# Kernel tuning notes

Hardware: AMD Instinct MI355X
Metric: run time of the kernel (lower is better)

The kernel has to match this reference:

```python
import jax, jax.numpy as jnp
import numpy as np

B, N, NB, P = 4, 2048, 10, 5
BIG = 1.0e5  # fill value for non-positive gt grasps


def _build_grasps(approach, base, contacts, thickness):
    # approach/base/contacts: [B,N,3], thickness: [B,N] -> [B,N,4,4]
    cross = jnp.cross(approach, base)
    R = jnp.stack([base, cross, approach], axis=-1)            # columns: [base, cross, approach]
    t = contacts + thickness[..., None] * 0.5 * base           # [B,N,3]
    top = jnp.concatenate([R, t[..., None]], axis=-1)          # [B,N,3,4]
    bottom = jnp.broadcast_to(jnp.array([0.0, 0.0, 0.0, 1.0], top.dtype),
                              top.shape[:-2] + (1, 4))
    return jnp.concatenate([top, bottom], axis=-2)             # [B,N,4,4]


def _transform_cps(cp_h, grasps):
    # cp_h: [P,4], grasps: [B,N,4,4] -> transformed control points [B,N,P,3]
    # torch: matmul(control_points, grasps^T)[..., :3]
    return jnp.einsum('pk,bnjk->bnpj', cp_h, grasps)[..., :3]


def _pairwise_sq(a, b):
    # a: [B,Na,P,3], b: [B,Nb,P,3] -> [B,Na,Nb] = sum_{p,c} (a-b)^2
    af = a.reshape(a.shape[0], a.shape[1], -1)
    bf = b.reshape(b.shape[0], b.shape[1], -1)
    a2 = jnp.sum(af * af, axis=-1)
    b2 = jnp.sum(bf * bf, axis=-1)
    d = a2[:, :, None] + b2[:, None, :] - 2.0 * jnp.einsum('bnd,bmd->bnm', af, bf)
    return jnp.maximum(d, 0.0)


def _forward(grasp_dir_head, approach_dir_head, grasp_offset_head, pred_points,
             binary_score_pred, binary_score_head, dir_labels_pc_cam, offset_labels_pc,
             grasp_success_labels_pc, approach_labels_pc_cam, bin_vals, bin_weights,
             control_pts, sym_control_pts):
    succ = grasp_success_labels_pc                              # [B,N] in {0,1}
    pos_in_view = jnp.maximum(jnp.sum(succ, axis=1), 1.0)       # min_geom_loss_divisor = 1.0

    # bin_offsets=True: lookup bin value of argmax bin
    thickness_pred = bin_vals[jnp.argmax(grasp_offset_head, axis=2)]   # [B,N]
    thickness_gt = bin_vals[jnp.argmax(offset_labels_pc, axis=2)]      # [B,N]

    pred_grasps = _build_grasps(approach_dir_head, grasp_dir_head, pred_points, thickness_pred)
    gt_grasps = _build_grasps(approach_labels_pc_cam, dir_labels_pc_cam, pred_points, thickness_gt)
    mask4 = succ.astype(bool)[:, :, None, None]
    pos_gt_grasps = jnp.where(mask4, gt_grasps, jnp.full_like(gt_grasps, BIG))

    ones_col = jnp.ones((P, 1), dtype=control_pts.dtype)
    cp_h = jnp.concatenate([control_pts, ones_col], axis=1)      # [P,4]
    scp_h = jnp.concatenate([sym_control_pts, ones_col], axis=1)

    pred_cp = _transform_cps(cp_h, pred_grasps)                  # [B,N,P,3]
    gt_cp_pos = _transform_cps(cp_h, pos_gt_grasps)
    sym_gt_cp_pos = _transform_cps(scp_h, pos_gt_grasps)

    # pred -> gt ADD-S (top-k with k=1 == min over concat of the two [B,N,N])
    d1 = _pairwise_sq(pred_cp, gt_cp_pos)
    d2 = _pairwise_sq(pred_cp, sym_gt_cp_pos)
    best = jnp.min(jnp.minimum(d1, d2), axis=2)                  # [B,N]
    gate = jnp.minimum(jnp.sum(succ, axis=1, keepdims=True), 1.0)
    min_adds = gate * jnp.sqrt(best)
    adds_loss = jnp.mean(binary_score_pred[:, :, 0] * min_adds)

    # gt -> pred ADD-S with unmasked gt grasps + confidence gather
    gt_cp = _transform_cps(cp_h, gt_grasps)
    sym_gt_cp = _transform_cps(scp_h, gt_grasps)
    dg1 = _pairwise_sq(gt_cp, pred_cp)                           # [B,Ngt,Npred]
    dg2 = _pairwise_sq(sym_gt_cp, pred_cp)
    m1 = jnp.min(dg1, axis=2); i1 = jnp.argmin(dg1, axis=2)
    m2 = jnp.min(dg2, axis=2); i2 = jnp.argmin(dg2, axis=2)
    # torch: where(-m1 < -m2, sym_idcs, idcs) == pick sym when m2 < m1
    idcs = jnp.where(m2 < m1, i2, i1)                            # [B,N]
    min_g2p = jnp.minimum(m1, m2) * succ
    conf = jnp.take_along_axis(binary_score_pred[:, :, 0], idcs, axis=1)
    adds_loss_gt2pred = jnp.mean(jnp.sum(conf * min_g2p, axis=1) / pos_in_view)

    # direction cosine loss
    cos_d = 1.0 - jnp.sum(dir_labels_pc_cam * grasp_dir_head, axis=2)
    dir_cosine_loss = jnp.mean(jnp.sum(cos_d * succ, axis=1) / pos_in_view)

    # approach cosine loss against orthogonalized label
    proj = jnp.sum(grasp_dir_head * approach_labels_pc_cam, axis=2, keepdims=True)
    orthog = approach_labels_pc_cam - proj * grasp_dir_head
    orthog = orthog / jnp.maximum(jnp.linalg.norm(orthog, axis=2, keepdims=True), 1e-12)
    cos_a = 1.0 - jnp.sum(orthog * approach_dir_head, axis=2)
    approach_cosine_loss = jnp.mean(jnp.sum(cos_a * succ, axis=1) / pos_in_view)

    # per-bin sigmoid BCE offset loss, bin-weighted
    bce = (offset_labels_pc * jax.nn.softplus(-grasp_offset_head)
           + (1.0 - offset_labels_pc) * jax.nn.softplus(grasp_offset_head))
    off = jnp.mean(bin_weights[None, None, :] * bce, axis=2)
    offset_loss = jnp.mean(jnp.sum(off * succ, axis=1) / pos_in_view)

    # binary success score BCE
    s = succ[:, :, None]
    score_bce = (s * jax.nn.softplus(-binary_score_head)
                 + (1.0 - s) * jax.nn.softplus(binary_score_head))
    bin_ce_loss = jnp.mean(score_bce)

    total = (1.0 * dir_cosine_loss + 1.0 * bin_ce_loss + 1.0 * offset_loss
             + 1.0 * approach_cosine_loss + 10.0 * adds_loss + 1.0 * adds_loss_gt2pred)
    return total


def setup_inputs():
    key = jax.random.key(0)
    ks = jax.random.split(key, 14)
    unit = lambda x: x / jnp.linalg.norm(x, axis=-1, keepdims=True)
    grasp_dir_head = unit(jax.random.normal(ks[0], (B, N, 3), jnp.float32))
    approach_dir_head = unit(jax.random.normal(ks[1], (B, N, 3), jnp.float32))
    grasp_offset_head = jax.random.normal(ks[2], (B, N, NB), jnp.float32)
    pred_points = jax.random.normal(ks[3], (B, N, 3), jnp.float32) * 0.3
    binary_score_pred = jax.random.uniform(ks[4], (B, N, 1), jnp.float32)
    binary_score_head = jax.random.normal(ks[5], (B, N, 1), jnp.float32)
    dir_labels_pc_cam = unit(jax.random.normal(ks[6], (B, N, 3), jnp.float32))
    offset_labels_pc = jax.nn.one_hot(jax.random.randint(ks[7], (B, N), 0, NB), NB, dtype=jnp.float32)
    grasp_success_labels_pc = jnp.round(jax.random.uniform(ks[8], (B, N), jnp.float32))
    approach_labels_pc_cam = unit(jax.random.normal(ks[9], (B, N, 3), jnp.float32))
    bin_vals = jnp.sort(jax.random.uniform(ks[10], (NB,), jnp.float32) * 0.075)
    bin_weights = jax.random.uniform(ks[11], (NB,), jnp.float32) + 0.5
    control_pts = jax.random.normal(ks[12], (P, 3), jnp.float32) * 0.05
    sym_control_pts = control_pts[jnp.array([0, 1, 3, 2, 4])]  # finger-swapped (symmetric) gripper
    return {
        'grasp_dir_head': grasp_dir_head,
        'approach_dir_head': approach_dir_head,
        'grasp_offset_head': grasp_offset_head,
        'pred_points': pred_points,
        'binary_score_pred': binary_score_pred,
        'binary_score_head': binary_score_head,
        'dir_labels_pc_cam': dir_labels_pc_cam,
        'offset_labels_pc': offset_labels_pc,
        'grasp_success_labels_pc': grasp_success_labels_pc,
        'approach_labels_pc_cam': approach_labels_pc_cam,
        'bin_vals': bin_vals,
        'bin_weights': bin_weights,
        'control_pts': control_pts,
        'sym_control_pts': sym_control_pts,
    }


def reference(grasp_dir_head, approach_dir_head, grasp_offset_head, pred_points,
              binary_score_pred, binary_score_head, dir_labels_pc_cam, offset_labels_pc,
              grasp_success_labels_pc, approach_labels_pc_cam, bin_vals, bin_weights,
              control_pts, sym_control_pts):
    return _forward(grasp_dir_head, approach_dir_head, grasp_offset_head, pred_points,
                    binary_score_pred, binary_score_head, dir_labels_pc_cam, offset_labels_pc,
                    grasp_success_labels_pc, approach_labels_pc_cam, bin_vals, bin_weights,
                    control_pts, sym_control_pts)
```

## Files before the change

### kernel.cpp

```cpp
#include <hip/hip_runtime.h>

#define Bn 4
#define Nn 2048
#define NBn 10
#define BN (Bn*Nn)
#define TM 64

#define OFF_PRED 0
#define OFF_GT   (BN*16)
#define OFF_SYM  (2*BN*16)
#define OFF_PN2  (3*BN*16)
#define OFF_GN2  (OFF_PN2 + BN)
#define OFF_SN2  (OFF_GN2 + BN)
#define OFF_BEST (OFF_SN2 + BN)
#define OFF_PK1  (OFF_BEST + BN)
#define OFF_PK2  (OFF_PK1 + 2*BN)
#define OFF_PART (OFF_PK2 + 2*BN)

__device__ inline float sp_(float x) {
  return fmaxf(x, 0.0f) + log1pf(expf(-fabsf(x)));
}

__device__ inline float dot16_(const float4&a0,const float4&a1,const float4&a2,const float4&a3,
                               const float4&b0,const float4&b1,const float4&b2,const float4&b3){
  float s0 = fmaf(a0.w,b0.w, fmaf(a0.z,b0.z, fmaf(a0.y,b0.y, a0.x*b0.x)));
  float s1 = fmaf(a1.w,b1.w, fmaf(a1.z,b1.z, fmaf(a1.y,b1.y, a1.x*b1.x)));
  float s2 = fmaf(a2.w,b2.w, fmaf(a2.z,b2.z, fmaf(a2.y,b2.y, a2.x*b2.x)));
  float s3 = fmaf(a3.w,b3.w, fmaf(a3.z,b3.z, fmaf(a3.y,b3.y, a3.x*b3.x)));
  return (s0+s1)+(s2+s3);
}

__device__ inline float blockSum_(float v, float* red) {
  #pragma unroll
  for (int o = 32; o > 0; o >>= 1) v += __shfl_down(v, o, 64);
  __syncthreads();
  if ((threadIdx.x & 63) == 0) red[threadIdx.x >> 6] = v;
  __syncthreads();
  return red[0] + red[1] + red[2] + red[3];
}

__global__ __launch_bounds__(64) void k_prep(
    const float* __restrict__ gdir, const float* __restrict__ adirp,
    const float* __restrict__ goff, const float* __restrict__ ppts,
    const float* __restrict__ dlab, const float* __restrict__ olab,
    const float* __restrict__ alab,
    const float* __restrict__ binv,
    const float* __restrict__ cpts, const float* __restrict__ scpts,
    float* __restrict__ ws)
{
  const int idx = blockIdx.x * 64 + threadIdx.x;

  const float gd0=gdir[idx*3+0],  gd1=gdir[idx*3+1],  gd2=gdir[idx*3+2];
  const float ad0=adirp[idx*3+0], ad1=adirp[idx*3+1], ad2=adirp[idx*3+2];
  const float dl0=dlab[idx*3+0],  dl1=dlab[idx*3+1],  dl2=dlab[idx*3+2];
  const float al0=alab[idx*3+0],  al1=alab[idx*3+1],  al2=alab[idx*3+2];
  const float pt0=ppts[idx*3+0],  pt1=ppts[idx*3+1],  pt2=ppts[idx*3+2];

  float bv = goff[idx*NBn]; int ap = 0;
  #pragma unroll
  for (int k = 1; k < NBn; k++) { float v = goff[idx*NBn+k]; if (v > bv) { bv = v; ap = k; } }
  float bg = olab[idx*NBn]; int ag = 0;
  #pragma unroll
  for (int k = 1; k < NBn; k++) { float v = olab[idx*NBn+k]; if (v > bg) { bg = v; ag = k; } }
  const float tp = binv[ap] * 0.5f;
  const float tg = binv[ag] * 0.5f;

  const float cp0 = ad1*gd2 - ad2*gd1, cp1 = ad2*gd0 - ad0*gd2, cp2 = ad0*gd1 - ad1*gd0;
  const float cg0 = al1*dl2 - al2*dl1, cg1 = al2*dl0 - al0*dl2, cg2 = al0*dl1 - al1*dl0;
  const float tpx = pt0 + tp*gd0, tpy = pt1 + tp*gd1, tpz = pt2 + tp*gd2;
  const float tgx = pt0 + tg*dl0, tgy = pt1 + tg*dl1, tgz = pt2 + tg*dl2;

  float pcp[15], gcp[15], hcp[15];
  float pn2 = 0.f, gn2 = 0.f, sn2 = 0.f;
  #pragma unroll
  for (int p = 0; p < 5; p++) {
    const float cx = cpts[p*3], cy = cpts[p*3+1], cz = cpts[p*3+2];
    const float sx = scpts[p*3], sy = scpts[p*3+1], sz = scpts[p*3+2];
    float x, y, z;
    x = gd0*cx + cp0*cy + ad0*cz + tpx;
    y = gd1*cx + cp1*cy + ad1*cz + tpy;
    z = gd2*cx + cp2*cy + ad2*cz + tpz;
    pcp[p*3+0]=x; pcp[p*3+1]=y; pcp[p*3+2]=z;
    pn2 = fmaf(x,x, fmaf(y,y, fmaf(z,z, pn2)));
    x = dl0*cx + cg0*cy + al0*cz + tgx;
    y = dl1*cx + cg1*cy + al1*cz + tgy;
    z = dl2*cx + cg2*cy + al2*cz + tgz;
    gcp[p*3+0]=x; gcp[p*3+1]=y; gcp[p*3+2]=z;
    gn2 = fmaf(x,x, fmaf(y,y, fmaf(z,z, gn2)));
    x = dl0*sx + cg0*sy + al0*sz + tgx;
    y = dl1*sx + cg1*sy + al1*sz + tgy;
    z = dl2*sx + cg2*sy + al2*sz + tgz;
    hcp[p*3+0]=x; hcp[p*3+1]=y; hcp[p*3+2]=z;
    sn2 = fmaf(x,x, fmaf(y,y, fmaf(z,z, sn2)));
  }

  float4* pd = (float4*)(ws + OFF_PRED) + (size_t)idx*4;
  pd[0]=make_float4(pcp[0],pcp[1],pcp[2],pcp[3]);
  pd[1]=make_float4(pcp[4],pcp[5],pcp[6],pcp[7]);
  pd[2]=make_float4(pcp[8],pcp[9],pcp[10],pcp[11]);
  pd[3]=make_float4(pcp[12],pcp[13],pcp[14],0.f);
  float4* gdst = (float4*)(ws + OFF_GT) + (size_t)idx*4;
  gdst[0]=make_float4(gcp[0],gcp[1],gcp[2],gcp[3]);
  gdst[1]=make_float4(gcp[4],gcp[5],gcp[6],gcp[7]);
  gdst[2]=make_float4(gcp[8],gcp[9],gcp[10],gcp[11]);
  gdst[3]=make_float4(gcp[12],gcp[13],gcp[14],0.f);
  float4* sdst = (float4*)(ws + OFF_SYM) + (size_t)idx*4;
  sdst[0]=make_float4(hcp[0],hcp[1],hcp[2],hcp[3]);
  sdst[1]=make_float4(hcp[4],hcp[5],hcp[6],hcp[7]);
  sdst[2]=make_float4(hcp[8],hcp[9],hcp[10],hcp[11]);
  sdst[3]=make_float4(hcp[12],hcp[13],hcp[14],0.f);
  ws[OFF_PN2+idx] = pn2; ws[OFF_GN2+idx] = gn2; ws[OFF_SN2+idx] = sn2;

  ((unsigned*)ws)[OFF_BEST + idx] = 0x7F800000u;
  ((unsigned long long*)(ws + OFF_PK1))[idx] = ~0ull;
  ((unsigned long long*)(ws + OFF_PK2))[idx] = ~0ull;
}

__global__ __launch_bounds__(256) void k_pair(const float* __restrict__ succ,
                                              float* __restrict__ ws) {
  __shared__ float4 gts[TM][4], sys[TM][4], prs[TM][4];
  __shared__ float gb2[TM], sb2[TM], pb2[TM], msk[TM];
  const int mt = blockIdx.x, nt = blockIdx.y, b = blockIdx.z;
  const int tid = threadIdx.x;
  const int r = tid >> 2, p = tid & 3;
  const int mrow = b*Nn + mt*TM + r;
  gts[r][p] = ((const float4*)(ws + OFF_GT))  [(size_t)mrow*4 + p];
  sys[r][p] = ((const float4*)(ws + OFF_SYM)) [(size_t)mrow*4 + p];
  prs[r][p] = ((const float4*)(ws + OFF_PRED))[(size_t)mrow*4 + p];
  if      (p == 0) gb2[r] = ws[OFF_GN2 + mrow];
  else if (p == 1) sb2[r] = ws[OFF_SN2 + mrow];
  else if (p == 2) pb2[r] = ws[OFF_PN2 + mrow];
  else             msk[r] = succ[mrow];
  __syncthreads();

  const int nrow = b*Nn + nt*256 + tid;
  const float INF = __int_as_float(0x7F800000);

  {
    const float4* pa = (const float4*)(ws + OFF_PRED) + (size_t)nrow*4;
    const float4 a0 = pa[0], a1 = pa[1], a2 = pa[2], a3 = pa[3];
    const float an2 = ws[OFF_PN2 + nrow];
    float best = INF;
    for (int m = 0; m < TM; m++) {
      if (msk[m] != 0.0f) {
        const float d1 = fmaxf(fmaf(-2.f, dot16_(a0,a1,a2,a3, gts[m][0],gts[m][1],gts[m][2],gts[m][3]), an2 + gb2[m]), 0.f);
        const float d2 = fmaxf(fmaf(-2.f, dot16_(a0,a1,a2,a3, sys[m][0],sys[m][1],sys[m][2],sys[m][3]), an2 + sb2[m]), 0.f);
        best = fminf(best, fminf(d1, d2));
      }
    }
    if (best < INF)
      atomicMin((unsigned int*)ws + OFF_BEST + nrow, __float_as_uint(best));
  }

  {
    const float4* g = (const float4*)(ws + OFF_GT)  + (size_t)nrow*4;
    const float4 g0=g[0], g1=g[1], g2=g[2], g3=g[3];
    const float4* s = (const float4*)(ws + OFF_SYM) + (size_t)nrow*4;
    const float4 s0=s[0], s1=s[1], s2=s[2], s3=s[3];
    const float gn2 = ws[OFF_GN2 + nrow], sn2 = ws[OFF_SN2 + nrow];
    unsigned long long b1 = ~0ull, b2 = ~0ull;
    for (int m = 0; m < TM; m++) {
      const float4 p0 = prs[m][0], p1 = prs[m][1], p2 = prs[m][2], p3 = prs[m][3];
      const float pb = pb2[m];
      const float d1 = fmaxf(fmaf(-2.f, dot16_(g0,g1,g2,g3,p0,p1,p2,p3), gn2 + pb), 0.f);
      const float d2 = fmaxf(fmaf(-2.f, dot16_(s0,s1,s2,s3,p0,p1,p2,p3), sn2 + pb), 0.f);
      const unsigned long long c1 = ((unsigned long long)__float_as_uint(d1) << 32) | (unsigned)(mt*TM + m);
      const unsigned long long c2 = ((unsigned long long)__float_as_uint(d2) << 32) | (unsigned)(mt*TM + m);
      b1 = (c1 < b1) ? c1 : b1;
      b2 = (c2 < b2) ? c2 : b2;
    }
    atomicMin((unsigned long long*)(ws + OFF_PK1) + nrow, b1);
    atomicMin((unsigned long long*)(ws + OFF_PK2) + nrow, b2);
  }
}

__global__ __launch_bounds__(256) void k_red(
    const float* __restrict__ bsp,  const float* __restrict__ bsh,
    const float* __restrict__ succ,
    const float* __restrict__ gdir, const float* __restrict__ adirp,
    const float* __restrict__ dlab, const float* __restrict__ alab,
    const float* __restrict__ goff, const float* __restrict__ olab,
    const float* __restrict__ binw,
    float* __restrict__ ws)
{
  __shared__ float red[4];
  const int b = blockIdx.y, nt = blockIdx.x;
  const int idx = b*Nn + nt*256 + threadIdx.x;
  const float sc = succ[idx];

  const float best = __uint_as_float(((const unsigned*)ws)[OFF_BEST + idx]);
  const float adds = (best < 1e30f) ? bsp[idx] * sqrtf(best) : 0.f;

  const unsigned long long p1 = ((const unsigned long long*)(ws + OFF_PK1))[idx];
  const unsigned long long p2 = ((const unsigned long long*)(ws + OFF_PK2))[idx];
  const float m1 = __uint_as_float((unsigned)(p1 >> 32));
  const float m2 = __uint_as_float((unsigned)(p2 >> 32));
  const int   i1 = (int)(p1 & 0xffffffffull);
  const int   i2 = (int)(p2 & 0xffffffffull);
  const int   id = (m2 < m1) ? i2 : i1;
  const float g2p = bsp[b*Nn + id] * fminf(m1, m2) * sc;

  const float gd0=gdir[idx*3+0],  gd1=gdir[idx*3+1],  gd2=gdir[idx*3+2];
  const float ad0=adirp[idx*3+0], ad1=adirp[idx*3+1], ad2=adirp[idx*3+2];
  const float dl0=dlab[idx*3+0],  dl1=dlab[idx*3+1],  dl2=dlab[idx*3+2];
  const float al0=alab[idx*3+0],  al1=alab[idx*3+1],  al2=alab[idx*3+2];

  const float cosd = 1.f - (dl0*gd0 + dl1*gd1 + dl2*gd2);
  const float proj = gd0*al0 + gd1*al1 + gd2*al2;
  const float o0 = al0 - proj*gd0, o1 = al1 - proj*gd1, o2 = al2 - proj*gd2;
  const float on = sqrtf(o0*o0 + o1*o1 + o2*o2);
  const float inv = 1.f / fmaxf(on, 1e-12f);
  const float cosa = 1.f - inv*(o0*ad0 + o1*ad1 + o2*ad2);

  float offv = 0.f;
  #pragma unroll
  for (int k = 0; k < NBn; k++) {
    const float x = goff[idx*NBn+k], lab = olab[idx*NBn+k];
    const float bce = lab * sp_(-x) + (1.f - lab) * sp_(x);
    offv = fmaf(binw[k], bce, offv);
  }
  offv *= (1.0f / NBn);
  const float sb = bsh[idx];
  const float sbce = sc * sp_(-sb) + (1.f - sc) * sp_(sb);

  float* part = ws + OFF_PART + (size_t)(b*8 + nt)*8;
  float t;
  t = blockSum_(cosd*sc, red); if (threadIdx.x == 0) part[0] = t;
  t = blockSum_(cosa*sc, red); if (threadIdx.x == 0) part[1] = t;
  t = blockSum_(offv*sc, red); if (threadIdx.x == 0) part[2] = t;
  t = blockSum_(sc, red);      if (threadIdx.x == 0) part[3] = t;
  t = blockSum_(sbce, red);    if (threadIdx.x == 0) part[4] = t;
  t = blockSum_(adds, red);    if (threadIdx.x == 0) part[5] = t;
  t = blockSum_(g2p, red);     if (threadIdx.x == 0) part[6] = t;
}

__global__ __launch_bounds__(64) void k_fin(const float* __restrict__ ws, float* __restrict__ out) {
  const int t = threadIdx.x;
  float v[7];
  #pragma unroll
  for (int c = 0; c < 7; c++) v[c] = (t < 32) ? ws[OFF_PART + t*8 + c] : 0.f;
  #pragma unroll
  for (int o = 1; o < 8; o <<= 1) {
    #pragma unroll
    for (int c = 0; c < 7; c++) v[c] += __shfl_xor(v[c], o, 64);
  }
  const float pos = fmaxf(v[3], 1.f);
  float vb   = (v[0] + v[1] + v[2] + v[6]) / pos;
  float bce  = v[4];
  float adds = v[5];
  #pragma unroll
  for (int o = 8; o < 32; o <<= 1) {
    vb   += __shfl_xor(vb,   o, 64);
    bce  += __shfl_xor(bce,  o, 64);
    adds += __shfl_xor(adds, o, 64);
  }
  if (t == 0)
    out[0] = vb * 0.25f + bce * (1.f/BN) + 10.f * adds * (1.f/BN);
}

extern "C" void kernel_launch(void* const* d_in, const int* in_sizes, int n_in,
                              void* d_out, int out_size, void* d_ws, size_t ws_size,
                              hipStream_t stream) {
  const float* gdir  = (const float*)d_in[0];
  const float* adirp = (const float*)d_in[1];
  const float* goff  = (const float*)d_in[2];
  const float* ppts  = (const float*)d_in[3];
  const float* bsp   = (const float*)d_in[4];
  const float* bsh   = (const float*)d_in[5];
  const float* dlab  = (const float*)d_in[6];
  const float* olab  = (const float*)d_in[7];
  const float* succ  = (const float*)d_in[8];
  const float* alab  = (const float*)d_in[9];
  const float* binv  = (const float*)d_in[10];
  const float* binw  = (const float*)d_in[11];
  const float* cpts  = (const float*)d_in[12];
  const float* scpts = (const float*)d_in[13];
  float* ws  = (float*)d_ws;
  float* out = (float*)d_out;

  k_prep<<<dim3(BN/64), dim3(64), 0, stream>>>(gdir, adirp, goff, ppts,
                                               dlab, olab, alab, binv, cpts, scpts, ws);
  k_pair<<<dim3(Nn/TM, Nn/256, Bn), dim3(256), 0, stream>>>(succ, ws);
  k_red<<<dim3(Nn/256, Bn), dim3(256), 0, stream>>>(bsp, bsh, succ, gdir, adirp,
                                                    dlab, alab, goff, olab, binw, ws);
  k_fin<<<1, 64, 0, stream>>>(ws, out);
}
```

Baseline: 136.4 us.

## Fuse pairwise min passes into one loop with packed 32-bit keys

The pairwise kernel now computes gt/sym versus pred distances once per pair and uses them for both reductions. The pred-side minimum is a wave-shuffle min with a large-bias mask for negative rows, and the gt-side argmin uses 32-bit keys that keep the top distance bits and store the index in the low bits. Per-point loss terms move from the reduce kernel into the prep kernel, leaving a slimmer final reduce. This halves the pairwise arithmetic and removes the 64-bit atomics. In exchange, distance precision in the argmin is truncated and tie-breaking may differ.

```diff
diff --git a/kernel.cpp b/kernel.cpp
--- a/kernel.cpp
+++ b/kernel.cpp
@@ -4,7 +4,9 @@
 #define Nn 2048
 #define NBn 10
 #define BN (Bn*Nn)
-#define TM 64
+#define TCOLS 128
+#define NCH 64
+#define BIGM 1e32f
 
 #define OFF_PRED 0
 #define OFF_GT   (BN*16)
@@ -13,20 +15,18 @@
 #define OFF_GN2  (OFF_PN2 + BN)
 #define OFF_SN2  (OFF_GN2 + BN)
 #define OFF_BEST (OFF_SN2 + BN)
-#define OFF_PK1  (OFF_BEST + BN)
-#define OFF_PK2  (OFF_PK1 + 2*BN)
-#define OFF_PART (OFF_PK2 + 2*BN)
+#define OFF_PK   (OFF_BEST + BN)
+#define OFF_PART (OFF_PK + BN)
 
 __device__ inline float sp_(float x) {
   return fmaxf(x, 0.0f) + log1pf(expf(-fabsf(x)));
 }
 
-__device__ inline float dot16_(const float4&a0,const float4&a1,const float4&a2,const float4&a3,
-                               const float4&b0,const float4&b1,const float4&b2,const float4&b3){
-  float s0 = fmaf(a0.w,b0.w, fmaf(a0.z,b0.z, fmaf(a0.y,b0.y, a0.x*b0.x)));
-  float s1 = fmaf(a1.w,b1.w, fmaf(a1.z,b1.z, fmaf(a1.y,b1.y, a1.x*b1.x)));
-  float s2 = fmaf(a2.w,b2.w, fmaf(a2.z,b2.z, fmaf(a2.y,b2.y, a2.x*b2.x)));
-  float s3 = fmaf(a3.w,b3.w, fmaf(a3.z,b3.z, fmaf(a3.y,b3.y, a3.x*b3.x)));
+__device__ inline float dotp_(const float* p, const float4&b0,const float4&b1,const float4&b2,const float4&b3){
+  float s0 = fmaf(p[3], b0.w, fmaf(p[2], b0.z, fmaf(p[1], b0.y, p[0]*b0.x)));
+  float s1 = fmaf(p[7], b1.w, fmaf(p[6], b1.z, fmaf(p[5], b1.y, p[4]*b1.x)));
+  float s2 = fmaf(p[11],b2.w, fmaf(p[10],b2.z, fmaf(p[9], b2.y, p[8]*b2.x)));
+  float s3 = fmaf(p[14],b3.z, fmaf(p[13],b3.y, p[12]*b3.x));
   return (s0+s1)+(s2+s3);
 }
 
@@ -39,22 +39,26 @@
   return red[0] + red[1] + red[2] + red[3];
 }
 
-__global__ __launch_bounds__(64) void k_prep(
+__global__ __launch_bounds__(256) void k_prep(
     const float* __restrict__ gdir, const float* __restrict__ adirp,
     const float* __restrict__ goff, const float* __restrict__ ppts,
+    const float* __restrict__ bsh,
     const float* __restrict__ dlab, const float* __restrict__ olab,
-    const float* __restrict__ alab,
-    const float* __restrict__ binv,
+    const float* __restrict__ succ, const float* __restrict__ alab,
+    const float* __restrict__ binv, const float* __restrict__ binw,
     const float* __restrict__ cpts, const float* __restrict__ scpts,
     float* __restrict__ ws)
 {
-  const int idx = blockIdx.x * 64 + threadIdx.x;
+  __shared__ float red[4];
+  const int pb = blockIdx.x;
+  const int idx = pb * 256 + threadIdx.x;
 
   const float gd0=gdir[idx*3+0],  gd1=gdir[idx*3+1],  gd2=gdir[idx*3+2];
   const float ad0=adirp[idx*3+0], ad1=adirp[idx*3+1], ad2=adirp[idx*3+2];
   const float dl0=dlab[idx*3+0],  dl1=dlab[idx*3+1],  dl2=dlab[idx*3+2];
   const float al0=alab[idx*3+0],  al1=alab[idx*3+1],  al2=alab[idx*3+2];
   const float pt0=ppts[idx*3+0],  pt1=ppts[idx*3+1],  pt2=ppts[idx*3+2];
+  const float sc = succ[idx];
 
   float bv = goff[idx*NBn]; int ap = 0;
   #pragma unroll
@@ -112,98 +116,7 @@
   ws[OFF_PN2+idx] = pn2; ws[OFF_GN2+idx] = gn2; ws[OFF_SN2+idx] = sn2;
 
   ((unsigned*)ws)[OFF_BEST + idx] = 0x7F800000u;
-  ((unsigned long long*)(ws + OFF_PK1))[idx] = ~0ull;
-  ((unsigned long long*)(ws + OFF_PK2))[idx] = ~0ull;
-}
-
-__global__ __launch_bounds__(256) void k_pair(const float* __restrict__ succ,
-                                              float* __restrict__ ws) {
-  __shared__ float4 gts[TM][4], sys[TM][4], prs[TM][4];
-  __shared__ float gb2[TM], sb2[TM], pb2[TM], msk[TM];
-  const int mt = blockIdx.x, nt = blockIdx.y, b = blockIdx.z;
-  const int tid = threadIdx.x;
-  const int r = tid >> 2, p = tid & 3;
-  const int mrow = b*Nn + mt*TM + r;
-  gts[r][p] = ((const float4*)(ws + OFF_GT))  [(size_t)mrow*4 + p];
-  sys[r][p] = ((const float4*)(ws + OFF_SYM)) [(size_t)mrow*4 + p];
-  prs[r][p] = ((const float4*)(ws + OFF_PRED))[(size_t)mrow*4 + p];
-  if      (p == 0) gb2[r] = ws[OFF_GN2 + mrow];
-  else if (p == 1) sb2[r] = ws[OFF_SN2 + mrow];
-  else if (p == 2) pb2[r] = ws[OFF_PN2 + mrow];
-  else             msk[r] = succ[mrow];
-  __syncthreads();
-
-  const int nrow = b*Nn + nt*256 + tid;
-  const float INF = __int_as_float(0x7F800000);
-
-  {
-    const float4* pa = (const float4*)(ws + OFF_PRED) + (size_t)nrow*4;
-    const float4 a0 = pa[0], a1 = pa[1], a2 = pa[2], a3 = pa[3];
-    const float an2 = ws[OFF_PN2 + nrow];
-    float best = INF;
-    for (int m = 0; m < TM; m++) {
-      if (msk[m] != 0.0f) {
-        const float d1 = fmaxf(fmaf(-2.f, dot16_(a0,a1,a2,a3, gts[m][0],gts[m][1],gts[m][2],gts[m][3]), an2 + gb2[m]), 0.f);
-        const float d2 = fmaxf(fmaf(-2.f, dot16_(a0,a1,a2,a3, sys[m][0],sys[m][1],sys[m][2],sys[m][3]), an2 + sb2[m]), 0.f);
-        best = fminf(best, fminf(d1, d2));
-      }
-    }
-    if (best < INF)
-      atomicMin((unsigned int*)ws + OFF_BEST + nrow, __float_as_uint(best));
-  }
-
-  {
-    const float4* g = (const float4*)(ws + OFF_GT)  + (size_t)nrow*4;
-    const float4 g0=g[0], g1=g[1], g2=g[2], g3=g[3];
-    const float4* s = (const float4*)(ws + OFF_SYM) + (size_t)nrow*4;
-    const float4 s0=s[0], s1=s[1], s2=s[2], s3=s[3];
-    const float gn2 = ws[OFF_GN2 + nrow], sn2 = ws[OFF_SN2 + nrow];
-    unsigned long long b1 = ~0ull, b2 = ~0ull;
-    for (int m = 0; m < TM; m++) {
-      const float4 p0 = prs[m][0], p1 = prs[m][1], p2 = prs[m][2], p3 = prs[m][3];
-      const float pb = pb2[m];
-      const float d1 = fmaxf(fmaf(-2.f, dot16_(g0,g1,g2,g3,p0,p1,p2,p3), gn2 + pb), 0.f);
-      const float d2 = fmaxf(fmaf(-2.f, dot16_(s0,s1,s2,s3,p0,p1,p2,p3), sn2 + pb), 0.f);
-      const unsigned long long c1 = ((unsigned long long)__float_as_uint(d1) << 32) | (unsigned)(mt*TM + m);
-      const unsigned long long c2 = ((unsigned long long)__float_as_uint(d2) << 32) | (unsigned)(mt*TM + m);
-      b1 = (c1 < b1) ? c1 : b1;
-      b2 = (c2 < b2) ? c2 : b2;
-    }
-    atomicMin((unsigned long long*)(ws + OFF_PK1) + nrow, b1);
-    atomicMin((unsigned long long*)(ws + OFF_PK2) + nrow, b2);
-  }
-}
-
-__global__ __launch_bounds__(256) void k_red(
-    const float* __restrict__ bsp,  const float* __restrict__ bsh,
-    const float* __restrict__ succ,
-    const float* __restrict__ gdir, const float* __restrict__ adirp,
-    const float* __restrict__ dlab, const float* __restrict__ alab,
-    const float* __restrict__ goff, const float* __restrict__ olab,
-    const float* __restrict__ binw,
-    float* __restrict__ ws)
-{
-  __shared__ float red[4];
-  const int b = blockIdx.y, nt = blockIdx.x;
-  const int idx = b*Nn + nt*256 + threadIdx.x;
-  const float sc = succ[idx];
-
-  const float best = __uint_as_float(((const unsigned*)ws)[OFF_BEST + idx]);
-  const float adds = (best < 1e30f) ? bsp[idx] * sqrtf(best) : 0.f;
-
-  const unsigned long long p1 = ((const unsigned long long*)(ws + OFF_PK1))[idx];
-  const unsigned long long p2 = ((const unsigned long long*)(ws + OFF_PK2))[idx];
-  const float m1 = __uint_as_float((unsigned)(p1 >> 32));
-  const float m2 = __uint_as_float((unsigned)(p2 >> 32));
-  const int   i1 = (int)(p1 & 0xffffffffull);
-  const int   i2 = (int)(p2 & 0xffffffffull);
-  const int   id = (m2 < m1) ? i2 : i1;
-  const float g2p = bsp[b*Nn + id] * fminf(m1, m2) * sc;
-
-  const float gd0=gdir[idx*3+0],  gd1=gdir[idx*3+1],  gd2=gdir[idx*3+2];
-  const float ad0=adirp[idx*3+0], ad1=adirp[idx*3+1], ad2=adirp[idx*3+2];
-  const float dl0=dlab[idx*3+0],  dl1=dlab[idx*3+1],  dl2=dlab[idx*3+2];
-  const float al0=alab[idx*3+0],  al1=alab[idx*3+1],  al2=alab[idx*3+2];
+  ((unsigned*)ws)[OFF_PK   + idx] = 0xFFFFFFFFu;
 
   const float cosd = 1.f - (dl0*gd0 + dl1*gd1 + dl2*gd2);
   const float proj = gd0*al0 + gd1*al1 + gd2*al2;
@@ -223,15 +136,98 @@
   const float sb = bsh[idx];
   const float sbce = sc * sp_(-sb) + (1.f - sc) * sp_(sb);
 
-  float* part = ws + OFF_PART + (size_t)(b*8 + nt)*8;
+  float* part = ws + OFF_PART + (size_t)pb*8;
   float t;
   t = blockSum_(cosd*sc, red); if (threadIdx.x == 0) part[0] = t;
   t = blockSum_(cosa*sc, red); if (threadIdx.x == 0) part[1] = t;
   t = blockSum_(offv*sc, red); if (threadIdx.x == 0) part[2] = t;
   t = blockSum_(sc, red);      if (threadIdx.x == 0) part[3] = t;
   t = blockSum_(sbce, red);    if (threadIdx.x == 0) part[4] = t;
-  t = blockSum_(adds, red);    if (threadIdx.x == 0) part[5] = t;
-  t = blockSum_(g2p, red);     if (threadIdx.x == 0) part[6] = t;
+}
+
+__global__ __launch_bounds__(256) void k_pair(const float* __restrict__ succ,
+                                              float* __restrict__ ws) {
+  __shared__ unsigned bkey[TCOLS];
+  const int tile = blockIdx.x * TCOLS, b = blockIdx.z;
+  const int bN = b * Nn;
+  const int tid = threadIdx.x;
+  const int lane = tid & 63;
+  const int wid = __builtin_amdgcn_readfirstlane(tid >> 6);
+
+  if (tid < TCOLS) bkey[tid] = 0xFFFFFFFFu;
+
+  const int r0 = bN + tile + lane;
+  const int r1 = r0 + 64;
+  const float4* G = (const float4*)(ws + OFF_GT);
+  const float4* S = (const float4*)(ws + OFF_SYM);
+  const float4 g00=G[(size_t)r0*4+0], g01=G[(size_t)r0*4+1], g02=G[(size_t)r0*4+2], g03=G[(size_t)r0*4+3];
+  const float4 g10=G[(size_t)r1*4+0], g11=G[(size_t)r1*4+1], g12=G[(size_t)r1*4+2], g13=G[(size_t)r1*4+3];
+  const float4 s00=S[(size_t)r0*4+0], s01=S[(size_t)r0*4+1], s02=S[(size_t)r0*4+2], s03=S[(size_t)r0*4+3];
+  const float4 s10=S[(size_t)r1*4+0], s11=S[(size_t)r1*4+1], s12=S[(size_t)r1*4+2], s13=S[(size_t)r1*4+3];
+  const float gn0 = ws[OFF_GN2+r0], gn1 = ws[OFF_GN2+r1];
+  const float sn0 = ws[OFF_SN2+r0], sn1 = ws[OFF_SN2+r1];
+  const float bias0 = (succ[r0] != 0.f) ? 0.f : BIGM;
+  const float bias1 = (succ[r1] != 0.f) ? 0.f : BIGM;
+
+  unsigned k0 = 0xFFFFFFFFu, k1 = 0xFFFFFFFFu;
+  __syncthreads();
+
+  const int nbase = blockIdx.y * NCH + wid * (NCH/4);
+  #pragma unroll 2
+  for (int j = 0; j < NCH/4; j++) {
+    const int n = nbase + j;
+    const float* pr = ws + OFF_PRED + (size_t)(bN + n)*16;
+    float p[15];
+    #pragma unroll
+    for (int q = 0; q < 15; q++) p[q] = pr[q];
+    const float pn2 = ws[OFF_PN2 + bN + n];
+
+    const float d10 = fmaxf(fmaf(-2.f, dotp_(p, g00,g01,g02,g03), pn2 + gn0), 0.f);
+    const float d20 = fmaxf(fmaf(-2.f, dotp_(p, s00,s01,s02,s03), pn2 + sn0), 0.f);
+    const float d11 = fmaxf(fmaf(-2.f, dotp_(p, g10,g11,g12,g13), pn2 + gn1), 0.f);
+    const float d21 = fmaxf(fmaf(-2.f, dotp_(p, s10,s11,s12,s13), pn2 + sn1), 0.f);
+
+    const unsigned nl = (unsigned)n, nh = (unsigned)n | 0x800u;
+    unsigned t0 = (__float_as_uint(d10) & 0xFFFFF000u) | nl;
+    unsigned t1 = (__float_as_uint(d20) & 0xFFFFF000u) | nh;
+    k0 = min(k0, min(t0, t1));
+    t0 = (__float_as_uint(d11) & 0xFFFFF000u) | nl;
+    t1 = (__float_as_uint(d21) & 0xFFFFF000u) | nh;
+    k1 = min(k1, min(t0, t1));
+
+    float f = fminf(fminf(d10, d20) + bias0, fminf(d11, d21) + bias1);
+    #pragma unroll
+    for (int o = 1; o < 64; o <<= 1) f = fminf(f, __shfl_xor(f, o, 64));
+    if (lane == 0)
+      atomicMin((unsigned*)ws + OFF_BEST + bN + n, __float_as_uint(f));
+  }
+
+  atomicMin(&bkey[lane], k0);
+  atomicMin(&bkey[64 + lane], k1);
+  __syncthreads();
+  if (tid < TCOLS)
+    atomicMin((unsigned*)ws + OFF_PK + bN + tile + tid, bkey[tid]);
+}
+
+__global__ __launch_bounds__(256) void k_red(const float* __restrict__ bsp,
+                                             const float* __restrict__ succ,
+                                             float* __restrict__ ws) {
+  __shared__ float red[4];
+  const int b = blockIdx.y, nt = blockIdx.x;
+  const int idx = b*Nn + nt*256 + threadIdx.x;
+
+  const float best = __uint_as_float(((const unsigned*)ws)[OFF_BEST + idx]);
+  const float adds = (best < 1e30f) ? bsp[idx] * sqrtf(best) : 0.f;
+
+  const unsigned key = ((const unsigned*)ws)[OFF_PK + idx];
+  const float d = __uint_as_float(key & 0xFFFFF000u);
+  const int  id = (int)(key & 0x7FFu);
+  const float g2p = bsp[b*Nn + id] * d * succ[idx];
+
+  float* part = ws + OFF_PART + (size_t)(b*8 + nt)*8;
+  float t;
+  t = blockSum_(adds, red); if (threadIdx.x == 0) part[5] = t;
+  t = blockSum_(g2p, red);  if (threadIdx.x == 0) part[6] = t;
 }
 
 __global__ __launch_bounds__(64) void k_fin(const float* __restrict__ ws, float* __restrict__ out) {
@@ -278,10 +274,10 @@
   float* ws  = (float*)d_ws;
   float* out = (float*)d_out;
 
-  k_prep<<<dim3(BN/64), dim3(64), 0, stream>>>(gdir, adirp, goff, ppts,
-                                               dlab, olab, alab, binv, cpts, scpts, ws);
-  k_pair<<<dim3(Nn/TM, Nn/256, Bn), dim3(256), 0, stream>>>(succ, ws);
-  k_red<<<dim3(Nn/256, Bn), dim3(256), 0, stream>>>(bsp, bsh, succ, gdir, adirp,
-                                                    dlab, alab, goff, olab, binw, ws);
+  k_prep<<<dim3(BN/256), dim3(256), 0, stream>>>(gdir, adirp, goff, ppts, bsh,
+                                                 dlab, olab, succ, alab,
+                                                 binv, binw, cpts, scpts, ws);
+  k_pair<<<dim3(Nn/TCOLS, Nn/NCH, Bn), dim3(256), 0, stream>>>(succ, ws);
+  k_red<<<dim3(Nn/256, Bn), dim3(256), 0, stream>>>(bsp, succ, ws);
   k_fin<<<1, 64, 0, stream>>>(ws, out);
 }
```

Result: no change. 139.2 us (+2.0%).
